# Kernel tuning notes

Hardware: AMD Instinct MI355X
Metric: run time of the kernel (lower is better)

The kernel has to match this reference:

```python
import jax, jax.numpy as jnp
import numpy as np

VOCAB = 8192
DIM = 64
COMMITMENT = 0.25
N = 65536


def setup_inputs() -> dict:
    key = jax.random.key(0)
    kx, ke = jax.random.split(key)
    x = jax.random.normal(kx, (N, DIM), dtype=jnp.float32)
    # matches nn.Embedding weight init uniform_(-0.5, 0.5)
    emb_weight = jax.random.uniform(ke, (VOCAB, DIM), dtype=jnp.float32, minval=-0.5, maxval=0.5)
    return {"x": x, "emb_weight": emb_weight}


def reference(x, emb_weight):
    # cdist(x, E, p=2): squared form gives identical argmin (sqrt is monotone)
    x2 = jnp.sum(x * x, axis=-1, keepdims=True)            # [N, 1]
    e2 = jnp.sum(emb_weight * emb_weight, axis=-1)         # [V]
    d2 = x2 + e2[None, :] - 2.0 * (x @ emb_weight.T)       # [N, V]
    idx = jnp.argmin(d2, axis=-1)                          # [N] int

    quantised = emb_weight[idx]                            # [N, D] gather

    codebook_loss = jnp.mean((quantised - jax.lax.stop_gradient(x)) ** 2)
    e_latent_loss = jnp.mean((jax.lax.stop_gradient(quantised) - x) ** 2)
    loss = codebook_loss + COMMITMENT * e_latent_loss

    # straight-through estimator
    quantised_ste = x + jax.lax.stop_gradient(quantised - x)
    return quantised_ste, loss, idx
```

## Files before the change

### kernel.cpp

```cpp
#include <hip/hip_runtime.h>

#define N 65536
#define D 64
#define V 8192
#define LOSS_OFF (N * D)
#define IDX_OFF (N * D + 1)
#define MARGIN 0.02f

typedef _Float16 half8 __attribute__((ext_vector_type(8)));
typedef float f32x4 __attribute__((ext_vector_type(4)));

typedef __attribute__((address_space(1))) const void gas_t;
typedef __attribute__((address_space(3))) void las_t;

#define DOT16(s, A0, A1, A2, A3, B0, B1, B2, B3)                         \
    s = fmaf(A0.x, B0.x, s); s = fmaf(A0.y, B0.y, s);                    \
    s = fmaf(A0.z, B0.z, s); s = fmaf(A0.w, B0.w, s);                    \
    s = fmaf(A1.x, B1.x, s); s = fmaf(A1.y, B1.y, s);                    \
    s = fmaf(A1.z, B1.z, s); s = fmaf(A1.w, B1.w, s);                    \
    s = fmaf(A2.x, B2.x, s); s = fmaf(A2.y, B2.y, s);                    \
    s = fmaf(A2.z, B2.z, s); s = fmaf(A2.w, B2.w, s);                    \
    s = fmaf(A3.x, B3.x, s); s = fmaf(A3.y, B3.y, s);                    \
    s = fmaf(A3.z, B3.z, s); s = fmaf(A3.w, B3.w, s);

__device__ __forceinline__ unsigned enc32(float f) {
    unsigned u = __float_as_uint(f);
    return (u & 0x80000000u) ? ~u : (u | 0x80000000u);
}

__global__ void k_split(const float* __restrict__ E, _Float16* __restrict__ Ef16,
                        float* __restrict__ e2, float* __restrict__ dout,
                        int* __restrict__ fcount) {
    int v = blockIdx.x * 256 + threadIdx.x;
    if (v == 0) {
        dout[LOSS_OFF] = 0.0f;
        *fcount = 0;
    }
    if (v >= V) return;
    const float4* row = (const float4*)(E + (size_t)v * D);
    float s = 0.0f;
#pragma unroll
    for (int i = 0; i < 16; ++i) {
        float4 t = row[i];
        s += t.x * t.x + t.y * t.y + t.z * t.z + t.w * t.w;
    }
    e2[v] = s;
#pragma unroll
    for (int i = 0; i < 8; ++i) {
        float4 lo = row[i * 2];
        float4 hi = row[i * 2 + 1];
        half8 h;
        h[0] = (_Float16)(-2.0f * lo.x); h[1] = (_Float16)(-2.0f * lo.y);
        h[2] = (_Float16)(-2.0f * lo.z); h[3] = (_Float16)(-2.0f * lo.w);
        h[4] = (_Float16)(-2.0f * hi.x); h[5] = (_Float16)(-2.0f * hi.y);
        h[6] = (_Float16)(-2.0f * hi.z); h[7] = (_Float16)(-2.0f * hi.w);
        *(half8*)(Ef16 + (size_t)v * D + i * 8) = h;
    }
}

#define MERGE(M1, M2, GID, L, PID)          \
    {                                       \
        bool bt = (L) < (M1);               \
        float m2c = bt ? (M1) : (L);        \
        (M2) = fminf((M2), m2c);            \
        (GID) = bt ? (PID) : (GID);         \
        (M1) = fminf((M1), (L));            \
    }

__global__ __launch_bounds__(256) void k_argmin(const float* __restrict__ X,
                                                const _Float16* __restrict__ Ef16,
                                                const float* __restrict__ e2,
                                                float4* __restrict__ part4) {
    __shared__ __align__(16) _Float16 els[2][8192];

    const int tid = threadIdx.x;
    const int lane = tid & 63;
    const int wave = tid >> 6;
    const int P = blockIdx.x & 1;
    const int rb = blockIdx.x >> 1;
    const int c4 = lane & 15;
    const int kg = lane >> 4;
    const int wrow = rb * 128 + wave * 32;
    const int sw = c4 & 7;
    const int k0off = (kg ^ sw) * 8;
    const int k1off = ((4 + kg) ^ sw) * 8;
    const int ch0 = P * 32;

    half8 x00, x01, x10, x11;
    {
        const float* xr0 = X + (size_t)(wrow + c4) * D;
        const float* xr1 = X + (size_t)(wrow + 16 + c4) * D;
#pragma unroll
        for (int f = 0; f < 2; ++f) {
            float4 lo = *(const float4*)(xr0 + f * 32 + kg * 8);
            float4 hi = *(const float4*)(xr0 + f * 32 + kg * 8 + 4);
            half8 h;
            h[0] = (_Float16)lo.x; h[1] = (_Float16)lo.y;
            h[2] = (_Float16)lo.z; h[3] = (_Float16)lo.w;
            h[4] = (_Float16)hi.x; h[5] = (_Float16)hi.y;
            h[6] = (_Float16)hi.z; h[7] = (_Float16)hi.w;
            if (f == 0) x00 = h; else x01 = h;
        }
#pragma unroll
        for (int f = 0; f < 2; ++f) {
            float4 lo = *(const float4*)(xr1 + f * 32 + kg * 8);
            float4 hi = *(const float4*)(xr1 + f * 32 + kg * 8 + 4);
            half8 h;
            h[0] = (_Float16)lo.x; h[1] = (_Float16)lo.y;
            h[2] = (_Float16)lo.z; h[3] = (_Float16)lo.w;
            h[4] = (_Float16)hi.x; h[5] = (_Float16)hi.y;
            h[6] = (_Float16)hi.z; h[7] = (_Float16)hi.w;
            if (f == 0) x10 = h; else x11 = h;
        }
    }

    const int q0 = tid, q1 = tid + 256, q2 = tid + 512, q3 = tid + 768;
    const _Float16* gs0 = Ef16 + (size_t)(ch0 * 128 + (q0 >> 3)) * 64 + ((q0 & 7) ^ ((q0 >> 3) & 7)) * 8;
    const _Float16* gs1 = Ef16 + (size_t)(ch0 * 128 + (q1 >> 3)) * 64 + ((q1 & 7) ^ ((q1 >> 3) & 7)) * 8;
    const _Float16* gs2 = Ef16 + (size_t)(ch0 * 128 + (q2 >> 3)) * 64 + ((q2 & 7) ^ ((q2 >> 3) & 7)) * 8;
    const _Float16* gs3 = Ef16 + (size_t)(ch0 * 128 + (q3 >> 3)) * 64 + ((q3 & 7) ^ ((q3 >> 3) & 7)) * 8;
    const int ld0 = q0 * 8, ld1 = q1 * 8, ld2 = q2 * 8, ld3 = q3 * 8;

#define STAGE(BUF)                                                            \
    {                                                                         \
        __builtin_amdgcn_global_load_lds((gas_t*)gs0, (las_t*)&els[BUF][ld0], 16, 0, 0); \
        __builtin_amdgcn_global_load_lds((gas_t*)gs1, (las_t*)&els[BUF][ld1], 16, 0, 0); \
        __builtin_amdgcn_global_load_lds((gas_t*)gs2, (las_t*)&els[BUF][ld2], 16, 0, 0); \
        __builtin_amdgcn_global_load_lds((gas_t*)gs3, (las_t*)&els[BUF][ld3], 16, 0, 0); \
        gs0 += 8192; gs1 += 8192; gs2 += 8192; gs3 += 8192;                   \
    }

    float m1a = 3.4e38f, m2a = 3.4e38f, m1b = 3.4e38f, m2b = 3.4e38f;
    unsigned gida = 0, gidb = 0;
    const unsigned kgu = (unsigned)kg;

#define TSTEP(T, E2Q)                                                         \
    {                                                                         \
        const half8 a0 = *(const half8*)&els[buf][(T * 16 + c4) * 64 + k0off];\
        const half8 a1 = *(const half8*)&els[buf][(T * 16 + c4) * 64 + k1off];\
        f32x4 acc0 = __builtin_amdgcn_mfma_f32_16x16x32_f16(a0, x00, E2Q, 0, 0, 0); \
        acc0 = __builtin_amdgcn_mfma_f32_16x16x32_f16(a1, x01, acc0, 0, 0, 0);\
        f32x4 acc1 = __builtin_amdgcn_mfma_f32_16x16x32_f16(a0, x10, E2Q, 0, 0, 0); \
        acc1 = __builtin_amdgcn_mfma_f32_16x16x32_f16(a1, x11, acc1, 0, 0, 0);\
        La = fminf(fminf(fminf(fminf(La, acc0[0]), acc0[1]), acc0[2]), acc0[3]); \
        Lb = fminf(fminf(fminf(fminf(Lb, acc1[0]), acc1[1]), acc1[2]), acc1[3]); \
    }

    STAGE(0)
    const f32x4* e2p = (const f32x4*)(e2 + (size_t)ch0 * 128) + kg;

    for (int ci = 0; ci < 32; ++ci) {
        __syncthreads();
        const f32x4 e2q0 = e2p[0],  e2q1 = e2p[4],  e2q2 = e2p[8],  e2q3 = e2p[12];
        const f32x4 e2q4 = e2p[16], e2q5 = e2p[20], e2q6 = e2p[24], e2q7 = e2p[28];
        e2p += 32;
        if (ci < 31) STAGE((ci + 1) & 1)
        const int buf = ci & 1;

        float La = 3.4e38f, Lb = 3.4e38f;
        TSTEP(0, e2q0) TSTEP(1, e2q1) TSTEP(2, e2q2) TSTEP(3, e2q3)
        TSTEP(4, e2q4) TSTEP(5, e2q5) TSTEP(6, e2q6) TSTEP(7, e2q7)

        unsigned pid = (unsigned)((ch0 + ci) * 4) + kgu;
        MERGE(m1a, m2a, gida, La, pid)
        MERGE(m1b, m2b, gidb, Lb, pid)
    }

#pragma unroll
    for (int off = 16; off < 64; off <<= 1) {
        float o1, o2;
        unsigned og;
        o1 = __shfl_xor(m1a, off, 64); o2 = __shfl_xor(m2a, off, 64);
        og = (unsigned)__shfl_xor((int)gida, off, 64);
        m2a = fminf(fminf(fmaxf(m1a, o1), m2a), o2);
        if (o1 < m1a) gida = og;
        m1a = fminf(m1a, o1);
        o1 = __shfl_xor(m1b, off, 64); o2 = __shfl_xor(m2b, off, 64);
        og = (unsigned)__shfl_xor((int)gidb, off, 64);
        m2b = fminf(fminf(fmaxf(m1b, o1), m2b), o2);
        if (o1 < m1b) gidb = og;
        m1b = fminf(m1b, o1);
    }

    if (lane < 16) {
        float4 r;
        r.x = m1a; r.y = m2a; r.z = __uint_as_float(gida); r.w = 0.0f;
        part4[(size_t)P * N + wrow + lane] = r;
        r.x = m1b; r.y = m2b; r.z = __uint_as_float(gidb);
        part4[(size_t)P * N + wrow + 16 + lane] = r;
    }
}

__global__ __launch_bounds__(256) void k_group(const float* __restrict__ X,
                                               const float* __restrict__ E,
                                               const float* __restrict__ e2,
                                               const float4* __restrict__ part4,
                                               unsigned* __restrict__ gidw,
                                               int* __restrict__ fcount,
                                               int* __restrict__ flist,
                                               unsigned long long* __restrict__ packed,
                                               float* __restrict__ dout) {
    const int lane = threadIdx.x & 63;
    const int row = blockIdx.x * 4 + (threadIdx.x >> 6);

    const float4 ra = part4[row];
    const float4 rbp = part4[N + row];
    const float m1a = ra.x, m2a = ra.y;
    const float m1b = rbp.x, m2b = rbp.y;
    const unsigned ga = __float_as_uint(ra.z);
    const unsigned gb = __float_as_uint(rbp.z);
    const float m1 = fminf(m1a, m1b);
    const float m2 = fminf(fminf(m2a, m2b), fmaxf(m1a, m1b));
    const unsigned g = (m1b < m1a) ? gb : ga;

    if (m2 - m1 < MARGIN) {
        if (lane == 0) {
            int p = atomicAdd(fcount, 1);
            flist[p] = row;
            packed[p] = ~0ull;
            gidw[row] = ((unsigned)p << 1) | 1u;
        }
        return;
    }
    if (lane == 0) gidw[row] = 0;

    const int ch = (int)(g >> 2);
    const int kgr = (int)(g & 3);
    const int e4 = lane >> 2;
    const int dg = lane & 3;
    const float4* xp = (const float4*)(X + (size_t)row * D) + dg * 4;
    float4 xa0 = xp[0], xa1 = xp[1], xa2 = xp[2], xa3 = xp[3];

    float best = 3.4e38f;
    int bidx = 0x7fffffff;
#pragma unroll
    for (int it = 0; it < 2; ++it) {
        const int s = it * 16 + e4;
        const int v = ch * 128 + ((s >> 2) << 4) + kgr * 4 + (s & 3);
        const float4* ep = (const float4*)(E + (size_t)v * D) + dg * 4;
        float4 b0 = ep[0], b1 = ep[1], b2 = ep[2], b3 = ep[3];
        float s0 = 0.0f;
        DOT16(s0, xa0, xa1, xa2, xa3, b0, b1, b2, b3)
        s0 += __shfl_xor(s0, 1, 64);
        s0 += __shfl_xor(s0, 2, 64);
        float d = fmaf(-2.0f, s0, e2[v]);
        if (d < best) { best = d; bidx = v; }
    }
#pragma unroll
    for (int off = 4; off < 64; off <<= 1) {
        float ob = __shfl_xor(best, off, 64);
        int oi = __shfl_xor(bidx, off, 64);
        if (ob < best || (ob == best && oi < bidx)) { best = ob; bidx = oi; }
    }
    if (lane == 0) dout[IDX_OFF + row] = (float)bidx;
}

__global__ __launch_bounds__(256) void k_full(const float* __restrict__ X,
                                              const float* __restrict__ E,
                                              const float* __restrict__ e2,
                                              const int* __restrict__ fcount,
                                              const int* __restrict__ flist,
                                              unsigned long long* __restrict__ packed) {
    const int nf = *fcount;
    if (nf == 0) return;
    const int nq = (nf + 3) >> 2;
    const int total = nq * 8;
    const int lane = threadIdx.x & 63;
    const int nwaves = gridDim.x * 4;
    int item = blockIdx.x * 4 + (threadIdx.x >> 6);
    const int e4 = lane >> 2;
    const int dg = lane & 3;

    for (; item < total; item += nwaves) {
        const int qi = item >> 3;
        const int c = item & 7;
        const int f0 = qi * 4;
        const int f1 = min(f0 + 1, nf - 1);
        const int f2 = min(f0 + 2, nf - 1);
        const int f3 = min(f0 + 3, nf - 1);
        const int r0 = flist[f0], r1 = flist[f1], r2 = flist[f2], r3 = flist[f3];

        const float4* xp0 = (const float4*)(X + (size_t)r0 * D) + dg * 4;
        const float4* xp1 = (const float4*)(X + (size_t)r1 * D) + dg * 4;
        const float4* xp2 = (const float4*)(X + (size_t)r2 * D) + dg * 4;
        const float4* xp3 = (const float4*)(X + (size_t)r3 * D) + dg * 4;
        float4 xa0 = xp0[0], xa1 = xp0[1], xa2 = xp0[2], xa3 = xp0[3];
        float4 xb0 = xp1[0], xb1 = xp1[1], xb2 = xp1[2], xb3 = xp1[3];
        float4 xc0 = xp2[0], xc1 = xp2[1], xc2 = xp2[2], xc3 = xp2[3];
        float4 xd0 = xp3[0], xd1 = xp3[1], xd2 = xp3[2], xd3 = xp3[3];

        unsigned long long k0 = ~0ull, k1 = ~0ull, k2 = ~0ull, k3 = ~0ull;

#pragma unroll 2
        for (int it = 0; it < 64; ++it) {
            const int v = c * 1024 + it * 16 + e4;
            const float4* ep = (const float4*)(E + (size_t)v * D) + dg * 4;
            float4 b0 = ep[0], b1 = ep[1], b2 = ep[2], b3 = ep[3];
            float s0 = 0.0f, s1 = 0.0f, s2 = 0.0f, s3 = 0.0f;
            DOT16(s0, xa0, xa1, xa2, xa3, b0, b1, b2, b3)
            DOT16(s1, xb0, xb1, xb2, xb3, b0, b1, b2, b3)
            DOT16(s2, xc0, xc1, xc2, xc3, b0, b1, b2, b3)
            DOT16(s3, xd0, xd1, xd2, xd3, b0, b1, b2, b3)
            s0 += __shfl_xor(s0, 1, 64); s0 += __shfl_xor(s0, 2, 64);
            s1 += __shfl_xor(s1, 1, 64); s1 += __shfl_xor(s1, 2, 64);
            s2 += __shfl_xor(s2, 1, 64); s2 += __shfl_xor(s2, 2, 64);
            s3 += __shfl_xor(s3, 1, 64); s3 += __shfl_xor(s3, 2, 64);
            const float ev = e2[v];
            const unsigned long long vb = (unsigned long long)(unsigned)v;
            unsigned long long t;
            t = ((unsigned long long)enc32(fmaf(-2.0f, s0, ev)) << 32) | vb;
            k0 = t < k0 ? t : k0;
            t = ((unsigned long long)enc32(fmaf(-2.0f, s1, ev)) << 32) | vb;
            k1 = t < k1 ? t : k1;
            t = ((unsigned long long)enc32(fmaf(-2.0f, s2, ev)) << 32) | vb;
            k2 = t < k2 ? t : k2;
            t = ((unsigned long long)enc32(fmaf(-2.0f, s3, ev)) << 32) | vb;
            k3 = t < k3 ? t : k3;
        }

#pragma unroll
        for (int off = 4; off < 64; off <<= 1) {
            unsigned lo, hi;
            unsigned long long o;
            lo = __shfl_xor((unsigned)k0, off, 64); hi = __shfl_xor((unsigned)(k0 >> 32), off, 64);
            o = ((unsigned long long)hi << 32) | lo; k0 = o < k0 ? o : k0;
            lo = __shfl_xor((unsigned)k1, off, 64); hi = __shfl_xor((unsigned)(k1 >> 32), off, 64);
            o = ((unsigned long long)hi << 32) | lo; k1 = o < k1 ? o : k1;
            lo = __shfl_xor((unsigned)k2, off, 64); hi = __shfl_xor((unsigned)(k2 >> 32), off, 64);
            o = ((unsigned long long)hi << 32) | lo; k2 = o < k2 ? o : k2;
            lo = __shfl_xor((unsigned)k3, off, 64); hi = __shfl_xor((unsigned)(k3 >> 32), off, 64);
            o = ((unsigned long long)hi << 32) | lo; k3 = o < k3 ? o : k3;
        }

        if (lane == 0) {
            atomicMin(&packed[f0], k0);
            atomicMin(&packed[f1], k1);
            atomicMin(&packed[f2], k2);
            atomicMin(&packed[f3], k3);
        }
    }
}

__global__ __launch_bounds__(256) void k_out(const float* __restrict__ X,
                                             const float* __restrict__ E,
                                             const unsigned* __restrict__ gidw,
                                             const unsigned long long* __restrict__ packed,
                                             float* __restrict__ dout) {
    float lsum = 0.0f;
    const int stride = gridDim.x * 256;
    for (int t = blockIdx.x * 256 + threadIdx.x; t < N * 16; t += stride) {
        const int n = t >> 4;
        const int d = (t & 15) * 4;
        const unsigned g = gidw[n];
        int idx;
        if (g & 1) {
            idx = (int)(unsigned)(packed[g >> 1] & 0xffffffffull);
            if (d == 0) dout[IDX_OFF + n] = (float)idx;
        } else {
            idx = (int)dout[IDX_OFF + n];
        }
        float4 x4 = *(const float4*)(X + (size_t)n * D + d);
        float4 q4 = *(const float4*)(E + (size_t)idx * D + d);
        float4 o;
        o.x = x4.x + (q4.x - x4.x);
        o.y = x4.y + (q4.y - x4.y);
        o.z = x4.z + (q4.z - x4.z);
        o.w = x4.w + (q4.w - x4.w);
        *(float4*)(dout + (size_t)n * D + d) = o;

        float dx = q4.x - x4.x, dy = q4.y - x4.y, dz = q4.z - x4.z,
              dw = q4.w - x4.w;
        lsum += dx * dx + dy * dy + dz * dz + dw * dw;
    }
#pragma unroll
    for (int off = 32; off; off >>= 1) lsum += __shfl_down(lsum, off, 64);
    __shared__ float ps[4];
    if ((threadIdx.x & 63) == 0) ps[threadIdx.x >> 6] = lsum;
    __syncthreads();
    if (threadIdx.x == 0) {
        float tot = ps[0] + ps[1] + ps[2] + ps[3];
        atomicAdd(dout + LOSS_OFF, tot * (1.25f / ((float)N * (float)D)));
    }
}

extern "C" void kernel_launch(void* const* d_in, const int* in_sizes, int n_in,
                              void* d_out, int out_size, void* d_ws,
                              size_t ws_size, hipStream_t stream) {
    const float* X = (const float*)d_in[0];
    const float* E = (const float*)d_in[1];
    float* out = (float*)d_out;

    char* ws = (char*)d_ws;
    _Float16* Ef16 = (_Float16*)ws;
    float* e2 = (float*)(ws + 1048576);
    unsigned* gidw = (unsigned*)(ws + 1081344);
    int* fcount = (int*)(ws + 1343488);
    int* flist = (int*)(ws + 1343744);
    unsigned long long* packed = (unsigned long long*)(ws + 1605888);
    float4* part4 = (float4*)(ws + 2130176);

    k_split<<<V / 256, 256, 0, stream>>>(E, Ef16, e2, out, fcount);
    k_argmin<<<(N / 128) * 2, 256, 0, stream>>>(X, Ef16, e2, part4);
    k_group<<<N / 4, 256, 0, stream>>>(X, E, e2, part4, gidw, fcount, flist, packed, out);
    k_full<<<1024, 256, 0, stream>>>(X, E, e2, fcount, flist, packed);
    k_out<<<512, 256, 0, stream>>>(X, E, gidw, packed, out);
}
```

Baseline: 210.7 us.

## Split argmin into 4 codebook partitions and fuse output writes into group kernel

The argmin kernel now uses 512-thread blocks covering 256 rows, and the codebook is split into four partitions of 16 chunks instead of two of 32. k_group merges the four partial results. For confident rows it also writes the straight-through output and a per-block partial loss directly, which removes the gidw indirection and the full pass over all rows in k_out. The new k_out2 handles only the fallback rows and sums the loss partials. k_split is parallelised to 8 threads per row. The costs are extra partial-result traffic and merge work in k_group.

```diff
diff --git a/kernel.cpp b/kernel.cpp
--- a/kernel.cpp
+++ b/kernel.cpp
@@ -6,6 +6,7 @@
 #define LOSS_OFF (N * D)
 #define IDX_OFF (N * D + 1)
 #define MARGIN 0.02f
+#define NPART 4
 
 typedef _Float16 half8 __attribute__((ext_vector_type(8)));
 typedef float f32x4 __attribute__((ext_vector_type(4)));
@@ -28,34 +29,32 @@
     return (u & 0x80000000u) ? ~u : (u | 0x80000000u);
 }
 
-__global__ void k_split(const float* __restrict__ E, _Float16* __restrict__ Ef16,
-                        float* __restrict__ e2, float* __restrict__ dout,
-                        int* __restrict__ fcount) {
-    int v = blockIdx.x * 256 + threadIdx.x;
-    if (v == 0) {
+__global__ __launch_bounds__(256) void k_split(const float* __restrict__ E,
+                                               _Float16* __restrict__ Ef16,
+                                               float* __restrict__ e2,
+                                               float* __restrict__ dout,
+                                               int* __restrict__ fcount) {
+    const int t = blockIdx.x * 256 + threadIdx.x;
+    if (t == 0) {
         dout[LOSS_OFF] = 0.0f;
         *fcount = 0;
     }
-    if (v >= V) return;
-    const float4* row = (const float4*)(E + (size_t)v * D);
-    float s = 0.0f;
-#pragma unroll
-    for (int i = 0; i < 16; ++i) {
-        float4 t = row[i];
-        s += t.x * t.x + t.y * t.y + t.z * t.z + t.w * t.w;
-    }
-    e2[v] = s;
-#pragma unroll
-    for (int i = 0; i < 8; ++i) {
-        float4 lo = row[i * 2];
-        float4 hi = row[i * 2 + 1];
-        half8 h;
-        h[0] = (_Float16)(-2.0f * lo.x); h[1] = (_Float16)(-2.0f * lo.y);
-        h[2] = (_Float16)(-2.0f * lo.z); h[3] = (_Float16)(-2.0f * lo.w);
-        h[4] = (_Float16)(-2.0f * hi.x); h[5] = (_Float16)(-2.0f * hi.y);
-        h[6] = (_Float16)(-2.0f * hi.z); h[7] = (_Float16)(-2.0f * hi.w);
-        *(half8*)(Ef16 + (size_t)v * D + i * 8) = h;
-    }
+    const int row = t >> 3;
+    const int seg = t & 7;
+    const float4* p = (const float4*)(E + (size_t)row * D + seg * 8);
+    float4 a = p[0], b = p[1];
+    float s = a.x * a.x + a.y * a.y + a.z * a.z + a.w * a.w +
+              b.x * b.x + b.y * b.y + b.z * b.z + b.w * b.w;
+    s += __shfl_xor(s, 1, 8);
+    s += __shfl_xor(s, 2, 8);
+    s += __shfl_xor(s, 4, 8);
+    if (seg == 0) e2[row] = s;
+    half8 h;
+    h[0] = (_Float16)(-2.0f * a.x); h[1] = (_Float16)(-2.0f * a.y);
+    h[2] = (_Float16)(-2.0f * a.z); h[3] = (_Float16)(-2.0f * a.w);
+    h[4] = (_Float16)(-2.0f * b.x); h[5] = (_Float16)(-2.0f * b.y);
+    h[6] = (_Float16)(-2.0f * b.z); h[7] = (_Float16)(-2.0f * b.w);
+    *(half8*)(Ef16 + (size_t)row * D + seg * 8) = h;
 }
 
 #define MERGE(M1, M2, GID, L, PID)          \
@@ -67,7 +66,7 @@
         (M1) = fminf((M1), (L));            \
     }
 
-__global__ __launch_bounds__(256) void k_argmin(const float* __restrict__ X,
+__global__ __launch_bounds__(512) void k_argmin(const float* __restrict__ X,
                                                 const _Float16* __restrict__ Ef16,
                                                 const float* __restrict__ e2,
                                                 float4* __restrict__ part4) {
@@ -76,15 +75,15 @@
     const int tid = threadIdx.x;
     const int lane = tid & 63;
     const int wave = tid >> 6;
-    const int P = blockIdx.x & 1;
-    const int rb = blockIdx.x >> 1;
+    const int P = blockIdx.x & 3;
+    const int rb = blockIdx.x >> 2;
     const int c4 = lane & 15;
     const int kg = lane >> 4;
-    const int wrow = rb * 128 + wave * 32;
+    const int wrow = rb * 256 + wave * 32;
     const int sw = c4 & 7;
     const int k0off = (kg ^ sw) * 8;
     const int k1off = ((4 + kg) ^ sw) * 8;
-    const int ch0 = P * 32;
+    const int ch0 = P * 16;
 
     half8 x00, x01, x10, x11;
     {
@@ -114,20 +113,16 @@
         }
     }
 
-    const int q0 = tid, q1 = tid + 256, q2 = tid + 512, q3 = tid + 768;
+    const int q0 = tid, q1 = tid + 512;
     const _Float16* gs0 = Ef16 + (size_t)(ch0 * 128 + (q0 >> 3)) * 64 + ((q0 & 7) ^ ((q0 >> 3) & 7)) * 8;
     const _Float16* gs1 = Ef16 + (size_t)(ch0 * 128 + (q1 >> 3)) * 64 + ((q1 & 7) ^ ((q1 >> 3) & 7)) * 8;
-    const _Float16* gs2 = Ef16 + (size_t)(ch0 * 128 + (q2 >> 3)) * 64 + ((q2 & 7) ^ ((q2 >> 3) & 7)) * 8;
-    const _Float16* gs3 = Ef16 + (size_t)(ch0 * 128 + (q3 >> 3)) * 64 + ((q3 & 7) ^ ((q3 >> 3) & 7)) * 8;
-    const int ld0 = q0 * 8, ld1 = q1 * 8, ld2 = q2 * 8, ld3 = q3 * 8;
+    const int ld0 = q0 * 8, ld1 = q1 * 8;
 
 #define STAGE(BUF)                                                            \
     {                                                                         \
         __builtin_amdgcn_global_load_lds((gas_t*)gs0, (las_t*)&els[BUF][ld0], 16, 0, 0); \
         __builtin_amdgcn_global_load_lds((gas_t*)gs1, (las_t*)&els[BUF][ld1], 16, 0, 0); \
-        __builtin_amdgcn_global_load_lds((gas_t*)gs2, (las_t*)&els[BUF][ld2], 16, 0, 0); \
-        __builtin_amdgcn_global_load_lds((gas_t*)gs3, (las_t*)&els[BUF][ld3], 16, 0, 0); \
-        gs0 += 8192; gs1 += 8192; gs2 += 8192; gs3 += 8192;                   \
+        gs0 += 8192; gs1 += 8192;                                             \
     }
 
     float m1a = 3.4e38f, m2a = 3.4e38f, m1b = 3.4e38f, m2b = 3.4e38f;
@@ -149,12 +144,12 @@
     STAGE(0)
     const f32x4* e2p = (const f32x4*)(e2 + (size_t)ch0 * 128) + kg;
 
-    for (int ci = 0; ci < 32; ++ci) {
+    for (int ci = 0; ci < 16; ++ci) {
         __syncthreads();
         const f32x4 e2q0 = e2p[0],  e2q1 = e2p[4],  e2q2 = e2p[8],  e2q3 = e2p[12];
         const f32x4 e2q4 = e2p[16], e2q5 = e2p[20], e2q6 = e2p[24], e2q7 = e2p[28];
         e2p += 32;
-        if (ci < 31) STAGE((ci + 1) & 1)
+        if (ci < 15) STAGE((ci + 1) & 1)
         const int buf = ci & 1;
 
         float La = 3.4e38f, Lb = 3.4e38f;
@@ -195,64 +190,93 @@
                                                const float* __restrict__ E,
                                                const float* __restrict__ e2,
                                                const float4* __restrict__ part4,
-                                               unsigned* __restrict__ gidw,
                                                int* __restrict__ fcount,
                                                int* __restrict__ flist,
                                                unsigned long long* __restrict__ packed,
+                                               float* __restrict__ lpart,
                                                float* __restrict__ dout) {
     const int lane = threadIdx.x & 63;
-    const int row = blockIdx.x * 4 + (threadIdx.x >> 6);
-
-    const float4 ra = part4[row];
-    const float4 rbp = part4[N + row];
-    const float m1a = ra.x, m2a = ra.y;
-    const float m1b = rbp.x, m2b = rbp.y;
-    const unsigned ga = __float_as_uint(ra.z);
-    const unsigned gb = __float_as_uint(rbp.z);
-    const float m1 = fminf(m1a, m1b);
-    const float m2 = fminf(fminf(m2a, m2b), fmaxf(m1a, m1b));
-    const unsigned g = (m1b < m1a) ? gb : ga;
-
+    const int wave = threadIdx.x >> 6;
+    const int row = blockIdx.x * 4 + wave;
+
+    float m1, m2;
+    unsigned g;
+    {
+        const float4 r0 = part4[row];
+        m1 = r0.x; m2 = r0.y; g = __float_as_uint(r0.z);
+#pragma unroll
+        for (int k = 1; k < NPART; ++k) {
+            const float4 r = part4[(size_t)k * N + row];
+            const unsigned rg = __float_as_uint(r.z);
+            if (r.x < m1) {
+                m2 = fminf(m2, m1);
+                m1 = r.x;
+                g = rg;
+            } else {
+                m2 = fminf(m2, r.x);
+            }
+            m2 = fminf(m2, r.y);
+        }
+    }
+
+    float lossp = 0.0f;
     if (m2 - m1 < MARGIN) {
         if (lane == 0) {
             int p = atomicAdd(fcount, 1);
             flist[p] = row;
             packed[p] = ~0ull;
-            gidw[row] = ((unsigned)p << 1) | 1u;
-        }
-        return;
-    }
-    if (lane == 0) gidw[row] = 0;
-
-    const int ch = (int)(g >> 2);
-    const int kgr = (int)(g & 3);
-    const int e4 = lane >> 2;
-    const int dg = lane & 3;
-    const float4* xp = (const float4*)(X + (size_t)row * D) + dg * 4;
-    float4 xa0 = xp[0], xa1 = xp[1], xa2 = xp[2], xa3 = xp[3];
-
-    float best = 3.4e38f;
-    int bidx = 0x7fffffff;
-#pragma unroll
-    for (int it = 0; it < 2; ++it) {
-        const int s = it * 16 + e4;
-        const int v = ch * 128 + ((s >> 2) << 4) + kgr * 4 + (s & 3);
-        const float4* ep = (const float4*)(E + (size_t)v * D) + dg * 4;
-        float4 b0 = ep[0], b1 = ep[1], b2 = ep[2], b3 = ep[3];
-        float s0 = 0.0f;
-        DOT16(s0, xa0, xa1, xa2, xa3, b0, b1, b2, b3)
-        s0 += __shfl_xor(s0, 1, 64);
-        s0 += __shfl_xor(s0, 2, 64);
-        float d = fmaf(-2.0f, s0, e2[v]);
-        if (d < best) { best = d; bidx = v; }
-    }
-#pragma unroll
-    for (int off = 4; off < 64; off <<= 1) {
-        float ob = __shfl_xor(best, off, 64);
-        int oi = __shfl_xor(bidx, off, 64);
-        if (ob < best || (ob == best && oi < bidx)) { best = ob; bidx = oi; }
-    }
-    if (lane == 0) dout[IDX_OFF + row] = (float)bidx;
+        }
+    } else {
+        const int ch = (int)(g >> 2);
+        const int kgr = (int)(g & 3);
+        const int e4 = lane >> 2;
+        const int dg = lane & 3;
+        const float4* xp = (const float4*)(X + (size_t)row * D) + dg * 4;
+        float4 xa0 = xp[0], xa1 = xp[1], xa2 = xp[2], xa3 = xp[3];
+
+        float best = 3.4e38f;
+        int bidx = 0x7fffffff;
+#pragma unroll
+        for (int it = 0; it < 2; ++it) {
+            const int s = it * 16 + e4;
+            const int v = ch * 128 + ((s >> 2) << 4) + kgr * 4 + (s & 3);
+            const float4* ep = (const float4*)(E + (size_t)v * D) + dg * 4;
+            float4 b0 = ep[0], b1 = ep[1], b2 = ep[2], b3 = ep[3];
+            float s0 = 0.0f;
+            DOT16(s0, xa0, xa1, xa2, xa3, b0, b1, b2, b3)
+            s0 += __shfl_xor(s0, 1, 64);
+            s0 += __shfl_xor(s0, 2, 64);
+            float d = fmaf(-2.0f, s0, e2[v]);
+            if (d < best) { best = d; bidx = v; }
+        }
+#pragma unroll
+        for (int off = 4; off < 64; off <<= 1) {
+            float ob = __shfl_xor(best, off, 64);
+            int oi = __shfl_xor(bidx, off, 64);
+            if (ob < best || (ob == best && oi < bidx)) { best = ob; bidx = oi; }
+        }
+        if (lane == 0) dout[IDX_OFF + row] = (float)bidx;
+        if (lane < 16) {
+            float4 x4 = *(const float4*)(X + (size_t)row * D + lane * 4);
+            float4 q4 = *(const float4*)(E + (size_t)bidx * D + lane * 4);
+            float4 o;
+            o.x = x4.x + (q4.x - x4.x);
+            o.y = x4.y + (q4.y - x4.y);
+            o.z = x4.z + (q4.z - x4.z);
+            o.w = x4.w + (q4.w - x4.w);
+            *(float4*)(dout + (size_t)row * D + lane * 4) = o;
+            float dx = q4.x - x4.x, dy = q4.y - x4.y, dz = q4.z - x4.z,
+                  dw = q4.w - x4.w;
+            lossp = dx * dx + dy * dy + dz * dz + dw * dw;
+        }
+    }
+
+#pragma unroll
+    for (int off = 32; off; off >>= 1) lossp += __shfl_down(lossp, off, 64);
+    __shared__ float ps[4];
+    if (lane == 0) ps[wave] = lossp;
+    __syncthreads();
+    if (threadIdx.x == 0) lpart[blockIdx.x] = ps[0] + ps[1] + ps[2] + ps[3];
 }
 
 __global__ __launch_bounds__(256) void k_full(const float* __restrict__ X,
@@ -341,41 +365,43 @@
     }
 }
 
-__global__ __launch_bounds__(256) void k_out(const float* __restrict__ X,
-                                             const float* __restrict__ E,
-                                             const unsigned* __restrict__ gidw,
-                                             const unsigned long long* __restrict__ packed,
-                                             float* __restrict__ dout) {
-    float lsum = 0.0f;
-    const int stride = gridDim.x * 256;
-    for (int t = blockIdx.x * 256 + threadIdx.x; t < N * 16; t += stride) {
-        const int n = t >> 4;
-        const int d = (t & 15) * 4;
-        const unsigned g = gidw[n];
-        int idx;
-        if (g & 1) {
-            idx = (int)(unsigned)(packed[g >> 1] & 0xffffffffull);
-            if (d == 0) dout[IDX_OFF + n] = (float)idx;
-        } else {
-            idx = (int)dout[IDX_OFF + n];
-        }
-        float4 x4 = *(const float4*)(X + (size_t)n * D + d);
-        float4 q4 = *(const float4*)(E + (size_t)idx * D + d);
-        float4 o;
-        o.x = x4.x + (q4.x - x4.x);
-        o.y = x4.y + (q4.y - x4.y);
-        o.z = x4.z + (q4.z - x4.z);
-        o.w = x4.w + (q4.w - x4.w);
-        *(float4*)(dout + (size_t)n * D + d) = o;
-
-        float dx = q4.x - x4.x, dy = q4.y - x4.y, dz = q4.z - x4.z,
-              dw = q4.w - x4.w;
-        lsum += dx * dx + dy * dy + dz * dz + dw * dw;
-    }
-#pragma unroll
-    for (int off = 32; off; off >>= 1) lsum += __shfl_down(lsum, off, 64);
+__global__ __launch_bounds__(256) void k_out2(const float* __restrict__ X,
+                                              const float* __restrict__ E,
+                                              const int* __restrict__ fcount,
+                                              const int* __restrict__ flist,
+                                              const unsigned long long* __restrict__ packed,
+                                              const float* __restrict__ lpart,
+                                              float* __restrict__ dout) {
+    const int lane = threadIdx.x & 63;
+    const int wave = threadIdx.x >> 6;
+    float lossp = 0.0f;
+    if (wave == 0) lossp += lpart[blockIdx.x * 64 + lane];
+
+    const int nf = *fcount;
+    const int nwaves = gridDim.x * 4;
+    for (int i = blockIdx.x * 4 + wave; i < nf; i += nwaves) {
+        const int row = flist[i];
+        const int idx = (int)(unsigned)(packed[i] & 0xffffffffull);
+        if (lane == 0) dout[IDX_OFF + row] = (float)idx;
+        if (lane < 16) {
+            float4 x4 = *(const float4*)(X + (size_t)row * D + lane * 4);
+            float4 q4 = *(const float4*)(E + (size_t)idx * D + lane * 4);
+            float4 o;
+            o.x = x4.x + (q4.x - x4.x);
+            o.y = x4.y + (q4.y - x4.y);
+            o.z = x4.z + (q4.z - x4.z);
+            o.w = x4.w + (q4.w - x4.w);
+            *(float4*)(dout + (size_t)row * D + lane * 4) = o;
+            float dx = q4.x - x4.x, dy = q4.y - x4.y, dz = q4.z - x4.z,
+                  dw = q4.w - x4.w;
+            lossp += dx * dx + dy * dy + dz * dz + dw * dw;
+        }
+    }
+
+#pragma unroll
+    for (int off = 32; off; off >>= 1) lossp += __shfl_down(lossp, off, 64);
     __shared__ float ps[4];
-    if ((threadIdx.x & 63) == 0) ps[threadIdx.x >> 6] = lsum;
+    if (lane == 0) ps[wave] = lossp;
     __syncthreads();
     if (threadIdx.x == 0) {
         float tot = ps[0] + ps[1] + ps[2] + ps[3];
@@ -393,15 +419,15 @@
     char* ws = (char*)d_ws;
     _Float16* Ef16 = (_Float16*)ws;
     float* e2 = (float*)(ws + 1048576);
-    unsigned* gidw = (unsigned*)(ws + 1081344);
-    int* fcount = (int*)(ws + 1343488);
-    int* flist = (int*)(ws + 1343744);
-    unsigned long long* packed = (unsigned long long*)(ws + 1605888);
-    float4* part4 = (float4*)(ws + 2130176);
-
-    k_split<<<V / 256, 256, 0, stream>>>(E, Ef16, e2, out, fcount);
-    k_argmin<<<(N / 128) * 2, 256, 0, stream>>>(X, Ef16, e2, part4);
-    k_group<<<N / 4, 256, 0, stream>>>(X, E, e2, part4, gidw, fcount, flist, packed, out);
+    int* fcount = (int*)(ws + 1081344);
+    int* flist = (int*)(ws + 1081600);
+    unsigned long long* packed = (unsigned long long*)(ws + 1343744);
+    float* lpart = (float*)(ws + 1868032);
+    float4* part4 = (float4*)(ws + 1933568);
+
+    k_split<<<256, 256, 0, stream>>>(E, Ef16, e2, out, fcount);
+    k_argmin<<<(N / 256) * NPART, 512, 0, stream>>>(X, Ef16, e2, part4);
+    k_group<<<N / 4, 256, 0, stream>>>(X, E, e2, part4, fcount, flist, packed, lpart, out);
     k_full<<<1024, 256, 0, stream>>>(X, E, e2, fcount, flist, packed);
-    k_out<<<512, 256, 0, stream>>>(X, E, gidw, packed, out);
-}
+    k_out2<<<256, 256, 0, stream>>>(X, E, fcount, flist, packed, lpart, out);
+}
```

Result: faster. 199.8 us (-5.2%).
